# Optimization experiments

Hardware: AMD Instinct MI355X
Metric: run time of the kernel (lower is better)

Reference implementation:

```python
import jax, jax.numpy as jnp
import numpy as np
import math

HEAD_DIM = 64
EMBED_DIM = 512
B, T = 16, 2048

def setup_inputs() -> dict:
    key = jax.random.key(0)
    k1, k2, k3 = jax.random.split(key, 3)
    x = jax.random.normal(k1, (B, T, EMBED_DIM), dtype=jnp.float32)
    # nn.Linear-style init scale
    s = 1.0 / math.sqrt(EMBED_DIM)
    Wq = jax.random.uniform(k2, (EMBED_DIM, HEAD_DIM), dtype=jnp.float32, minval=-s, maxval=s)
    bq = jax.random.uniform(k3, (HEAD_DIM,), dtype=jnp.float32, minval=-s, maxval=s)
    return {"x": x, "Wq": Wq, "bq": bq}

def reference(x, Wq, bq):
    # Faithful to source: q, k, v all come from the SAME query projection.
    q = jnp.einsum('bte,ed->btd', x, Wq) + bq  # [B,T,D]
    d_k = q.shape[-1]
    # weights[b, i, j] = q_i . q_j / sqrt(d_k)
    weights = jnp.einsum('bid,bjd->bij', q, q) / jnp.sqrt(jnp.float32(d_k))
    # NOTE: source applies softmax over dim=1 (query/row axis), not dim=-1.
    weights = jax.nn.softmax(weights, axis=1)
    attention = jnp.einsum('bij,bjd->bid', weights, q)  # v == q in source
    return attention
```

## Files before the change

kernel.cpp:

```cpp
#include <hip/hip_runtime.h>
#include <hip/hip_bf16.h>

#define BN 16
#define TN 2048
#define DN 64
#define EN 512
#define PAD 68

using f32x4  = __attribute__((ext_vector_type(4))) float;
using bf16x8 = __attribute__((ext_vector_type(8))) short;
using bf16x4 = __attribute__((ext_vector_type(4))) short;

static __device__ __forceinline__ short f2bf(float f) {
    __hip_bfloat16 h = __float2bfloat16(f);
    return __builtin_bit_cast(short, h);
}
static __device__ __forceinline__ float bf2f(short s) {
    return __bfloat162float(__builtin_bit_cast(__hip_bfloat16, s));
}

__global__ __launch_bounds__(256) void wprep_kernel(
    const float* __restrict__ Wq, short* __restrict__ WTh,
    short* __restrict__ WTl)
{
    __shared__ float wlds[64][65];
    const int tid = threadIdx.x;
    const int k0 = blockIdx.x * 64;
    #pragma unroll
    for (int it = 0; it < 16; ++it) {
        int idx = it * 256 + tid;
        int k = idx >> 6, n = idx & 63;
        wlds[k][n] = Wq[(size_t)(k0 + k) * 64 + n];
    }
    __syncthreads();
    #pragma unroll
    for (int it = 0; it < 16; ++it) {
        int idx = it * 256 + tid;
        int n = idx >> 6, k = idx & 63;
        float v = wlds[k][n];
        short h = f2bf(v);
        short l = f2bf(v - bf2f(h));
        WTh[(size_t)n * EN + k0 + k] = h;
        WTl[(size_t)n * EN + k0 + k] = l;
    }
}

__global__ __launch_bounds__(256, 2) void qproj_kernel(
    const float* __restrict__ x, const short* __restrict__ WTh,
    const short* __restrict__ WTl, const float* __restrict__ bq,
    short* __restrict__ Qb, short* __restrict__ QTb)
{
    __shared__ short xh[64 * 40];
    __shared__ short wth[64 * 40];
    __shared__ short wtl[64 * 40];
    __shared__ short tl[64][68];

    const int tid = threadIdx.x;
    const int lane = tid & 63;
    const int wv = tid >> 6;
    const int c = lane & 15;
    const int g = lane >> 4;
    const int rowbase = blockIdx.x * 64;
    const int b = rowbase >> 11;
    const int tbase = rowbase & (TN - 1);

    const int sr = tid >> 3;
    const int sc4 = tid & 7;

    float4 xa = *reinterpret_cast<const float4*>(&x[(size_t)(rowbase + sr) * EN + sc4 * 4]);
    float4 xb = *reinterpret_cast<const float4*>(&x[(size_t)(rowbase + 32 + sr) * EN + sc4 * 4]);
    bf16x4 wa = *reinterpret_cast<const bf16x4*>(&WTh[(size_t)sr * EN + sc4 * 4]);
    bf16x4 wb = *reinterpret_cast<const bf16x4*>(&WTh[(size_t)(32 + sr) * EN + sc4 * 4]);
    bf16x4 la = *reinterpret_cast<const bf16x4*>(&WTl[(size_t)sr * EN + sc4 * 4]);
    bf16x4 lb = *reinterpret_cast<const bf16x4*>(&WTl[(size_t)(32 + sr) * EN + sc4 * 4]);

    f32x4 acc[4];
    #pragma unroll
    for (int nt = 0; nt < 4; ++nt) acc[nt] = (f32x4){0.f, 0.f, 0.f, 0.f};

    for (int ks = 0; ks < EN; ks += 32) {
        __syncthreads();
        bf16x4 h0, h1;
        #pragma unroll
        for (int j = 0; j < 4; ++j) { h0[j] = f2bf(xa[j]); h1[j] = f2bf(xb[j]); }
        *reinterpret_cast<bf16x4*>(&xh[sr * 40 + sc4 * 4]) = h0;
        *reinterpret_cast<bf16x4*>(&xh[(32 + sr) * 40 + sc4 * 4]) = h1;
        *reinterpret_cast<bf16x4*>(&wth[sr * 40 + sc4 * 4]) = wa;
        *reinterpret_cast<bf16x4*>(&wth[(32 + sr) * 40 + sc4 * 4]) = wb;
        *reinterpret_cast<bf16x4*>(&wtl[sr * 40 + sc4 * 4]) = la;
        *reinterpret_cast<bf16x4*>(&wtl[(32 + sr) * 40 + sc4 * 4]) = lb;

        const int kn = (ks + 32 < EN) ? ks + 32 : ks;
        xa = *reinterpret_cast<const float4*>(&x[(size_t)(rowbase + sr) * EN + kn + sc4 * 4]);
        xb = *reinterpret_cast<const float4*>(&x[(size_t)(rowbase + 32 + sr) * EN + kn + sc4 * 4]);
        wa = *reinterpret_cast<const bf16x4*>(&WTh[(size_t)sr * EN + kn + sc4 * 4]);
        wb = *reinterpret_cast<const bf16x4*>(&WTh[(size_t)(32 + sr) * EN + kn + sc4 * 4]);
        la = *reinterpret_cast<const bf16x4*>(&WTl[(size_t)sr * EN + kn + sc4 * 4]);
        lb = *reinterpret_cast<const bf16x4*>(&WTl[(size_t)(32 + sr) * EN + kn + sc4 * 4]);
        __syncthreads();

        bf16x8 av = *reinterpret_cast<const bf16x8*>(&xh[(wv * 16 + c) * 40 + g * 8]);
        #pragma unroll
        for (int nt = 0; nt < 4; ++nt) {
            bf16x8 bh = *reinterpret_cast<const bf16x8*>(&wth[(nt * 16 + c) * 40 + g * 8]);
            bf16x8 bl = *reinterpret_cast<const bf16x8*>(&wtl[(nt * 16 + c) * 40 + g * 8]);
            acc[nt] = __builtin_amdgcn_mfma_f32_16x16x32_bf16(av, bh, acc[nt], 0, 0, 0);
            acc[nt] = __builtin_amdgcn_mfma_f32_16x16x32_bf16(av, bl, acc[nt], 0, 0, 0);
        }
    }

    __syncthreads();
    #pragma unroll
    for (int nt = 0; nt < 4; ++nt) {
        const float bias = bq[nt * 16 + c];
        #pragma unroll
        for (int r = 0; r < 4; ++r) {
            const int row = wv * 16 + g * 4 + r;
            short qb = f2bf(acc[nt][r] + bias);
            Qb[(size_t)(rowbase + row) * DN + nt * 16 + c] = qb;
            tl[nt * 16 + c][row] = qb;
        }
    }
    __syncthreads();
    #pragma unroll
    for (int it = 0; it < 4; ++it) {
        int idx = it * 256 + tid;
        int d = idx >> 4;
        int j4 = (idx & 15) * 4;
        *reinterpret_cast<short4*>(&QTb[((size_t)(b * 64 + d)) * TN + tbase + j4]) =
            *reinterpret_cast<const short4*>(&tl[d][j4]);
    }
}

__global__ __launch_bounds__(256, 4) void stats_kernel(
    const short* __restrict__ Qb, float* __restrict__ l_part)
{
    __shared__ short Qt[64 * PAD];
    const int tid = threadIdx.x;
    const int lane = tid & 63;
    const int wv = tid >> 6;
    const int c = lane & 15;
    const int g = lane >> 4;
    const int b = blockIdx.y;
    const int z = blockIdx.z;
    const int jbase = blockIdx.x * 64 + wv * 16;
    const short* Qbb = Qb + (size_t)b * TN * DN;

    bf16x8 a0 = *reinterpret_cast<const bf16x8*>(Qbb + (size_t)(jbase + c) * DN + g * 8);
    bf16x8 a1 = *reinterpret_cast<const bf16x8*>(Qbb + (size_t)(jbase + c) * DN + g * 8 + 32);

    const int srow = tid >> 2;
    const int schk = tid & 3;
    const int ilo = z * (TN / 2);

    bf16x8 v0 = *reinterpret_cast<const bf16x8*>(Qbb + (size_t)(ilo + srow) * DN + schk * 16);
    bf16x8 v1 = *reinterpret_cast<const bf16x8*>(Qbb + (size_t)(ilo + srow) * DN + schk * 16 + 8);

    float l[4] = {0.f, 0.f, 0.f, 0.f};
    for (int ii = 0; ii < TN / 2; ii += 64) {
        __syncthreads();
        *reinterpret_cast<bf16x8*>(&Qt[srow * PAD + schk * 16]) = v0;
        *reinterpret_cast<bf16x8*>(&Qt[srow * PAD + schk * 16 + 8]) = v1;
        const int in_ = ilo + ((ii + 64 < TN / 2) ? ii + 64 : ii);
        v0 = *reinterpret_cast<const bf16x8*>(Qbb + (size_t)(in_ + srow) * DN + schk * 16);
        v1 = *reinterpret_cast<const bf16x8*>(Qbb + (size_t)(in_ + srow) * DN + schk * 16 + 8);
        __syncthreads();

        #pragma unroll
        for (int it = 0; it < 4; ++it) {
            bf16x8 b0 = *reinterpret_cast<const bf16x8*>(&Qt[(it * 16 + c) * PAD + g * 8]);
            bf16x8 b1 = *reinterpret_cast<const bf16x8*>(&Qt[(it * 16 + c) * PAD + g * 8 + 32]);
            f32x4 acc = {0.f, 0.f, 0.f, 0.f};
            acc = __builtin_amdgcn_mfma_f32_16x16x32_bf16(a0, b0, acc, 0, 0, 0);
            acc = __builtin_amdgcn_mfma_f32_16x16x32_bf16(a1, b1, acc, 0, 0, 0);
            #pragma unroll
            for (int r = 0; r < 4; ++r)
                l[r] += __expf(acc[r] * 0.125f);
        }
    }
    #pragma unroll
    for (int r = 0; r < 4; ++r) {
        float v = l[r];
        v += __shfl_xor(v, 1);
        v += __shfl_xor(v, 2);
        v += __shfl_xor(v, 4);
        v += __shfl_xor(v, 8);
        l[r] = v;
    }
    if (c == 0) {
        #pragma unroll
        for (int r = 0; r < 4; ++r)
            l_part[((size_t)z * BN + b) * TN + jbase + g * 4 + r] = l[r];
    }
}

__global__ __launch_bounds__(256) void fuse_kernel(
    const short* __restrict__ QTb, const float* __restrict__ l_part,
    short* __restrict__ RT)
{
    const int idx = blockIdx.x * 256 + threadIdx.x;
    const int c8 = idx & 255;
    const int bd = idx >> 8;
    const int b = bd >> 6;
    const int j0 = c8 * 8;

    bf16x8 q = *reinterpret_cast<const bf16x8*>(&QTb[(size_t)bd * TN + j0]);
    const float* lp0 = l_part + (size_t)b * TN + j0;
    const float* lp1 = l_part + (size_t)(BN + b) * TN + j0;
    bf16x8 r;
    #pragma unroll
    for (int t = 0; t < 8; ++t)
        r[t] = f2bf(bf2f(q[t]) / (lp0[t] + lp1[t]));
    *reinterpret_cast<bf16x8*>(&RT[(size_t)bd * TN + j0]) = r;
}

__global__ __launch_bounds__(256, 4) void pv_kernel(
    const short* __restrict__ Qb, const short* __restrict__ RT,
    float* __restrict__ out0, float* __restrict__ out1)
{
    __shared__ short Qt[64 * PAD];
    __shared__ short RTt[64 * PAD];
    __shared__ short Pt[4][16 * PAD];

    const int tid = threadIdx.x;
    const int lane = tid & 63;
    const int wv = tid >> 6;
    const int c = lane & 15;
    const int g = lane >> 4;
    const int b = blockIdx.y;
    const int z = blockIdx.z;
    const int ibase = blockIdx.x * 64 + wv * 16;
    const short* Qbb = Qb + (size_t)b * TN * DN;
    const short* RTb = RT + (size_t)b * DN * TN;

    bf16x8 bi0 = *reinterpret_cast<const bf16x8*>(Qbb + (size_t)(ibase + c) * DN + g * 8);
    bf16x8 bi1 = *reinterpret_cast<const bf16x8*>(Qbb + (size_t)(ibase + c) * DN + g * 8 + 32);

    f32x4 o[4];
    #pragma unroll
    for (int dt = 0; dt < 4; ++dt) o[dt] = (f32x4){0.f, 0.f, 0.f, 0.f};

    const int srow = tid >> 2;
    const int schk = tid & 3;
    const int jlo = z * (TN / 2);

    bf16x8 vq0 = *reinterpret_cast<const bf16x8*>(Qbb + (size_t)(jlo + srow) * DN + schk * 16);
    bf16x8 vq1 = *reinterpret_cast<const bf16x8*>(Qbb + (size_t)(jlo + srow) * DN + schk * 16 + 8);
    bf16x8 vt0 = *reinterpret_cast<const bf16x8*>(RTb + (size_t)srow * TN + jlo + schk * 16);
    bf16x8 vt1 = *reinterpret_cast<const bf16x8*>(RTb + (size_t)srow * TN + jlo + schk * 16 + 8);

    for (int jj = 0; jj < TN / 2; jj += 64) {
        __syncthreads();
        *reinterpret_cast<bf16x8*>(&Qt[srow * PAD + schk * 16]) = vq0;
        *reinterpret_cast<bf16x8*>(&Qt[srow * PAD + schk * 16 + 8]) = vq1;
        *reinterpret_cast<bf16x8*>(&RTt[srow * PAD + schk * 16]) = vt0;
        *reinterpret_cast<bf16x8*>(&RTt[srow * PAD + schk * 16 + 8]) = vt1;

        const int jn = jlo + ((jj + 64 < TN / 2) ? jj + 64 : jj);
        vq0 = *reinterpret_cast<const bf16x8*>(Qbb + (size_t)(jn + srow) * DN + schk * 16);
        vq1 = *reinterpret_cast<const bf16x8*>(Qbb + (size_t)(jn + srow) * DN + schk * 16 + 8);
        vt0 = *reinterpret_cast<const bf16x8*>(RTb + (size_t)srow * TN + jn + schk * 16);
        vt1 = *reinterpret_cast<const bf16x8*>(RTb + (size_t)srow * TN + jn + schk * 16 + 8);
        __syncthreads();

        bf16x8 aq[4][2];
        #pragma unroll
        for (int dt = 0; dt < 4; ++dt) {
            aq[dt][0] = *reinterpret_cast<const bf16x8*>(&RTt[(dt * 16 + c) * PAD + g * 8]);
            aq[dt][1] = *reinterpret_cast<const bf16x8*>(&RTt[(dt * 16 + c) * PAD + 32 + g * 8]);
        }

        #pragma unroll
        for (int jt = 0; jt < 4; ++jt) {
            bf16x8 a0 = *reinterpret_cast<const bf16x8*>(&Qt[(jt * 16 + c) * PAD + g * 8]);
            bf16x8 a1 = *reinterpret_cast<const bf16x8*>(&Qt[(jt * 16 + c) * PAD + g * 8 + 32]);
            f32x4 accs = {0.f, 0.f, 0.f, 0.f};
            accs = __builtin_amdgcn_mfma_f32_16x16x32_bf16(a0, bi0, accs, 0, 0, 0);
            accs = __builtin_amdgcn_mfma_f32_16x16x32_bf16(a1, bi1, accs, 0, 0, 0);
            bf16x4 pw;
            #pragma unroll
            for (int r = 0; r < 4; ++r)
                pw[r] = f2bf(__expf(accs[r] * 0.125f));
            *reinterpret_cast<bf16x4*>(&Pt[wv][c * PAD + jt * 16 + g * 4]) = pw;
        }
        asm volatile("s_waitcnt lgkmcnt(0)" ::: "memory");
        __builtin_amdgcn_sched_barrier(0);

        bf16x8 p0 = *reinterpret_cast<const bf16x8*>(&Pt[wv][c * PAD + g * 8]);
        bf16x8 p1 = *reinterpret_cast<const bf16x8*>(&Pt[wv][c * PAD + 32 + g * 8]);
        #pragma unroll
        for (int dt = 0; dt < 4; ++dt) {
            o[dt] = __builtin_amdgcn_mfma_f32_16x16x32_bf16(aq[dt][0], p0, o[dt], 0, 0, 0);
            o[dt] = __builtin_amdgcn_mfma_f32_16x16x32_bf16(aq[dt][1], p1, o[dt], 0, 0, 0);
        }
    }

    float* outb = (z ? out1 : out0) + (size_t)b * TN * DN;
    #pragma unroll
    for (int dt = 0; dt < 4; ++dt) {
        float4 v4;
        v4.x = o[dt][0]; v4.y = o[dt][1]; v4.z = o[dt][2]; v4.w = o[dt][3];
        *reinterpret_cast<float4*>(&outb[(size_t)(ibase + c) * DN + dt * 16 + g * 4]) = v4;
    }
}

__global__ __launch_bounds__(256) void reduce_kernel(
    float* __restrict__ out, const float* __restrict__ part1)
{
    const size_t i = (size_t)blockIdx.x * 256 + threadIdx.x;
    float4 a = reinterpret_cast<float4*>(out)[i];
    float4 b = reinterpret_cast<const float4*>(part1)[i];
    a.x += b.x; a.y += b.y; a.z += b.z; a.w += b.w;
    reinterpret_cast<float4*>(out)[i] = a;
}

extern "C" void kernel_launch(void* const* d_in, const int* in_sizes, int n_in,
                              void* d_out, int out_size, void* d_ws, size_t ws_size,
                              hipStream_t stream) {
    const float* x  = (const float*)d_in[0];
    const float* Wq = (const float*)d_in[1];
    const float* bq = (const float*)d_in[2];
    float* out = (float*)d_out;

    short* Qb   = (short*)d_ws;
    short* QTb  = Qb + (size_t)BN * TN * DN;
    short* RT   = QTb + (size_t)BN * TN * DN;
    float* lpar = (float*)(RT + (size_t)BN * TN * DN);
    short* WTh  = (short*)(lpar + (size_t)2 * BN * TN);
    short* WTl  = WTh + (size_t)DN * EN;
    float* part1 = (float*)(WTl + (size_t)DN * EN);

    wprep_kernel<<<dim3(EN / 64), dim3(256), 0, stream>>>(Wq, WTh, WTl);
    qproj_kernel<<<dim3(BN * TN / 64), dim3(256), 0, stream>>>(x, WTh, WTl, bq, Qb, QTb);
    stats_kernel<<<dim3(TN / 64, BN, 2), dim3(256), 0, stream>>>(Qb, lpar);
    fuse_kernel<<<dim3(BN * DN * TN / 8 / 256), dim3(256), 0, stream>>>(QTb, lpar, RT);
    pv_kernel<<<dim3(TN / 64, BN, 2), dim3(256), 0, stream>>>(Qb, RT, out, part1);
    reduce_kernel<<<dim3(BN * TN * DN / 4 / 256), dim3(256), 0, stream>>>(out, part1);
}
```

Measured before the change: 82.49 us.

## Double-buffer qproj LDS, fold exp scale into Q, split stats four ways

The Q projection kernel now double-buffers its LDS tiles, so each k-step needs one barrier instead of two, and global loads are issued two steps ahead. The 1/sqrt(d)*log2(e) factor is folded into the stored Qb so the exponentials become plain exp2 with no multiply. The stats kernel is split four ways along the sum axis to give more blocks, and the fuse kernel now sums four partial denominators. __syncthreads is replaced by a lighter lgkmcnt wait plus s_barrier. This adds LDS use and partial-sum traffic, and rounding Q after scaling changes numerics slightly.

```diff
diff --git a/kernel.cpp b/kernel.cpp
--- a/kernel.cpp
+++ b/kernel.cpp
@@ -6,6 +6,7 @@
 #define DN 64
 #define EN 512
 #define PAD 68
+#define SQK 0.42466084f
 
 using f32x4  = __attribute__((ext_vector_type(4))) float;
 using bf16x8 = __attribute__((ext_vector_type(8))) short;
@@ -17,6 +18,10 @@
 }
 static __device__ __forceinline__ float bf2f(short s) {
     return __bfloat162float(__builtin_bit_cast(__hip_bfloat16, s));
+}
+static __device__ __forceinline__ void bar_lds() {
+    asm volatile("s_waitcnt lgkmcnt(0)" ::: "memory");
+    __builtin_amdgcn_s_barrier();
 }
 
 __global__ __launch_bounds__(256) void wprep_kernel(
@@ -50,9 +55,9 @@
     const short* __restrict__ WTl, const float* __restrict__ bq,
     short* __restrict__ Qb, short* __restrict__ QTb)
 {
-    __shared__ short xh[64 * 40];
-    __shared__ short wth[64 * 40];
-    __shared__ short wtl[64 * 40];
+    __shared__ short xh[2 * 64 * 40];
+    __shared__ short wth[2 * 64 * 40];
+    __shared__ short wtl[2 * 64 * 40];
     __shared__ short tl[64][68];
 
     const int tid = threadIdx.x;
@@ -66,20 +71,21 @@
 
     const int sr = tid >> 3;
     const int sc4 = tid & 7;
-
-    float4 xa = *reinterpret_cast<const float4*>(&x[(size_t)(rowbase + sr) * EN + sc4 * 4]);
-    float4 xb = *reinterpret_cast<const float4*>(&x[(size_t)(rowbase + 32 + sr) * EN + sc4 * 4]);
-    bf16x4 wa = *reinterpret_cast<const bf16x4*>(&WTh[(size_t)sr * EN + sc4 * 4]);
-    bf16x4 wb = *reinterpret_cast<const bf16x4*>(&WTh[(size_t)(32 + sr) * EN + sc4 * 4]);
-    bf16x4 la = *reinterpret_cast<const bf16x4*>(&WTl[(size_t)sr * EN + sc4 * 4]);
-    bf16x4 lb = *reinterpret_cast<const bf16x4*>(&WTl[(size_t)(32 + sr) * EN + sc4 * 4]);
-
-    f32x4 acc[4];
-    #pragma unroll
-    for (int nt = 0; nt < 4; ++nt) acc[nt] = (f32x4){0.f, 0.f, 0.f, 0.f};
-
-    for (int ks = 0; ks < EN; ks += 32) {
-        __syncthreads();
+    const size_t xr0 = (size_t)(rowbase + sr) * EN + sc4 * 4;
+    const size_t xr1 = (size_t)(rowbase + 32 + sr) * EN + sc4 * 4;
+    const size_t wr0 = (size_t)sr * EN + sc4 * 4;
+    const size_t wr1 = (size_t)(32 + sr) * EN + sc4 * 4;
+
+    float4 xa, xb;
+    bf16x4 wa, wb, la, lb;
+
+    xa = *reinterpret_cast<const float4*>(&x[xr0]);
+    xb = *reinterpret_cast<const float4*>(&x[xr1]);
+    wa = *reinterpret_cast<const bf16x4*>(&WTh[wr0]);
+    wb = *reinterpret_cast<const bf16x4*>(&WTh[wr1]);
+    la = *reinterpret_cast<const bf16x4*>(&WTl[wr0]);
+    lb = *reinterpret_cast<const bf16x4*>(&WTl[wr1]);
+    {
         bf16x4 h0, h1;
         #pragma unroll
         for (int j = 0; j < 4; ++j) { h0[j] = f2bf(xa[j]); h1[j] = f2bf(xb[j]); }
@@ -89,24 +95,53 @@
         *reinterpret_cast<bf16x4*>(&wth[(32 + sr) * 40 + sc4 * 4]) = wb;
         *reinterpret_cast<bf16x4*>(&wtl[sr * 40 + sc4 * 4]) = la;
         *reinterpret_cast<bf16x4*>(&wtl[(32 + sr) * 40 + sc4 * 4]) = lb;
-
-        const int kn = (ks + 32 < EN) ? ks + 32 : ks;
-        xa = *reinterpret_cast<const float4*>(&x[(size_t)(rowbase + sr) * EN + kn + sc4 * 4]);
-        xb = *reinterpret_cast<const float4*>(&x[(size_t)(rowbase + 32 + sr) * EN + kn + sc4 * 4]);
-        wa = *reinterpret_cast<const bf16x4*>(&WTh[(size_t)sr * EN + kn + sc4 * 4]);
-        wb = *reinterpret_cast<const bf16x4*>(&WTh[(size_t)(32 + sr) * EN + kn + sc4 * 4]);
-        la = *reinterpret_cast<const bf16x4*>(&WTl[(size_t)sr * EN + kn + sc4 * 4]);
-        lb = *reinterpret_cast<const bf16x4*>(&WTl[(size_t)(32 + sr) * EN + kn + sc4 * 4]);
-        __syncthreads();
-
-        bf16x8 av = *reinterpret_cast<const bf16x8*>(&xh[(wv * 16 + c) * 40 + g * 8]);
+    }
+    xa = *reinterpret_cast<const float4*>(&x[xr0 + 32]);
+    xb = *reinterpret_cast<const float4*>(&x[xr1 + 32]);
+    wa = *reinterpret_cast<const bf16x4*>(&WTh[wr0 + 32]);
+    wb = *reinterpret_cast<const bf16x4*>(&WTh[wr1 + 32]);
+    la = *reinterpret_cast<const bf16x4*>(&WTl[wr0 + 32]);
+    lb = *reinterpret_cast<const bf16x4*>(&WTl[wr1 + 32]);
+    bar_lds();
+
+    f32x4 acc[4];
+    #pragma unroll
+    for (int nt = 0; nt < 4; ++nt) acc[nt] = (f32x4){0.f, 0.f, 0.f, 0.f};
+
+    for (int t = 0; t < 16; ++t) {
+        const int cur = t & 1;
+        const int co = cur * 2560;
+        if (t + 1 < 16) {
+            const int wo = (cur ^ 1) * 2560;
+            bf16x4 h0, h1;
+            #pragma unroll
+            for (int j = 0; j < 4; ++j) { h0[j] = f2bf(xa[j]); h1[j] = f2bf(xb[j]); }
+            *reinterpret_cast<bf16x4*>(&xh[wo + sr * 40 + sc4 * 4]) = h0;
+            *reinterpret_cast<bf16x4*>(&xh[wo + (32 + sr) * 40 + sc4 * 4]) = h1;
+            *reinterpret_cast<bf16x4*>(&wth[wo + sr * 40 + sc4 * 4]) = wa;
+            *reinterpret_cast<bf16x4*>(&wth[wo + (32 + sr) * 40 + sc4 * 4]) = wb;
+            *reinterpret_cast<bf16x4*>(&wtl[wo + sr * 40 + sc4 * 4]) = la;
+            *reinterpret_cast<bf16x4*>(&wtl[wo + (32 + sr) * 40 + sc4 * 4]) = lb;
+        }
+        if (t + 2 < 16) {
+            const int kn = (t + 2) * 32;
+            xa = *reinterpret_cast<const float4*>(&x[xr0 + kn]);
+            xb = *reinterpret_cast<const float4*>(&x[xr1 + kn]);
+            wa = *reinterpret_cast<const bf16x4*>(&WTh[wr0 + kn]);
+            wb = *reinterpret_cast<const bf16x4*>(&WTh[wr1 + kn]);
+            la = *reinterpret_cast<const bf16x4*>(&WTl[wr0 + kn]);
+            lb = *reinterpret_cast<const bf16x4*>(&WTl[wr1 + kn]);
+        }
+
+        bf16x8 av = *reinterpret_cast<const bf16x8*>(&xh[co + (wv * 16 + c) * 40 + g * 8]);
         #pragma unroll
         for (int nt = 0; nt < 4; ++nt) {
-            bf16x8 bh = *reinterpret_cast<const bf16x8*>(&wth[(nt * 16 + c) * 40 + g * 8]);
-            bf16x8 bl = *reinterpret_cast<const bf16x8*>(&wtl[(nt * 16 + c) * 40 + g * 8]);
+            bf16x8 bh = *reinterpret_cast<const bf16x8*>(&wth[co + (nt * 16 + c) * 40 + g * 8]);
+            bf16x8 bl = *reinterpret_cast<const bf16x8*>(&wtl[co + (nt * 16 + c) * 40 + g * 8]);
             acc[nt] = __builtin_amdgcn_mfma_f32_16x16x32_bf16(av, bh, acc[nt], 0, 0, 0);
             acc[nt] = __builtin_amdgcn_mfma_f32_16x16x32_bf16(av, bl, acc[nt], 0, 0, 0);
         }
+        bar_lds();
     }
 
     __syncthreads();
@@ -116,9 +151,9 @@
         #pragma unroll
         for (int r = 0; r < 4; ++r) {
             const int row = wv * 16 + g * 4 + r;
-            short qb = f2bf(acc[nt][r] + bias);
-            Qb[(size_t)(rowbase + row) * DN + nt * 16 + c] = qb;
-            tl[nt * 16 + c][row] = qb;
+            const float q = acc[nt][r] + bias;
+            Qb[(size_t)(rowbase + row) * DN + nt * 16 + c] = f2bf(q * SQK);
+            tl[nt * 16 + c][row] = f2bf(q);
         }
     }
     __syncthreads();
@@ -151,20 +186,20 @@
 
     const int srow = tid >> 2;
     const int schk = tid & 3;
-    const int ilo = z * (TN / 2);
+    const int ilo = z * (TN / 4);
 
     bf16x8 v0 = *reinterpret_cast<const bf16x8*>(Qbb + (size_t)(ilo + srow) * DN + schk * 16);
     bf16x8 v1 = *reinterpret_cast<const bf16x8*>(Qbb + (size_t)(ilo + srow) * DN + schk * 16 + 8);
 
     float l[4] = {0.f, 0.f, 0.f, 0.f};
-    for (int ii = 0; ii < TN / 2; ii += 64) {
-        __syncthreads();
+    for (int ii = 0; ii < TN / 4; ii += 64) {
+        bar_lds();
         *reinterpret_cast<bf16x8*>(&Qt[srow * PAD + schk * 16]) = v0;
         *reinterpret_cast<bf16x8*>(&Qt[srow * PAD + schk * 16 + 8]) = v1;
-        const int in_ = ilo + ((ii + 64 < TN / 2) ? ii + 64 : ii);
+        const int in_ = ilo + ((ii + 64 < TN / 4) ? ii + 64 : ii);
         v0 = *reinterpret_cast<const bf16x8*>(Qbb + (size_t)(in_ + srow) * DN + schk * 16);
         v1 = *reinterpret_cast<const bf16x8*>(Qbb + (size_t)(in_ + srow) * DN + schk * 16 + 8);
-        __syncthreads();
+        bar_lds();
 
         #pragma unroll
         for (int it = 0; it < 4; ++it) {
@@ -175,7 +210,7 @@
             acc = __builtin_amdgcn_mfma_f32_16x16x32_bf16(a1, b1, acc, 0, 0, 0);
             #pragma unroll
             for (int r = 0; r < 4; ++r)
-                l[r] += __expf(acc[r] * 0.125f);
+                l[r] += __builtin_exp2f(acc[r]);
         }
     }
     #pragma unroll
@@ -207,10 +242,12 @@
     bf16x8 q = *reinterpret_cast<const bf16x8*>(&QTb[(size_t)bd * TN + j0]);
     const float* lp0 = l_part + (size_t)b * TN + j0;
     const float* lp1 = l_part + (size_t)(BN + b) * TN + j0;
+    const float* lp2 = l_part + (size_t)(2 * BN + b) * TN + j0;
+    const float* lp3 = l_part + (size_t)(3 * BN + b) * TN + j0;
     bf16x8 r;
     #pragma unroll
     for (int t = 0; t < 8; ++t)
-        r[t] = f2bf(bf2f(q[t]) / (lp0[t] + lp1[t]));
+        r[t] = f2bf(bf2f(q[t]) / (lp0[t] + lp1[t] + lp2[t] + lp3[t]));
     *reinterpret_cast<bf16x8*>(&RT[(size_t)bd * TN + j0]) = r;
 }
 
@@ -250,7 +287,7 @@
     bf16x8 vt1 = *reinterpret_cast<const bf16x8*>(RTb + (size_t)srow * TN + jlo + schk * 16 + 8);
 
     for (int jj = 0; jj < TN / 2; jj += 64) {
-        __syncthreads();
+        bar_lds();
         *reinterpret_cast<bf16x8*>(&Qt[srow * PAD + schk * 16]) = vq0;
         *reinterpret_cast<bf16x8*>(&Qt[srow * PAD + schk * 16 + 8]) = vq1;
         *reinterpret_cast<bf16x8*>(&RTt[srow * PAD + schk * 16]) = vt0;
@@ -261,7 +298,7 @@
         vq1 = *reinterpret_cast<const bf16x8*>(Qbb + (size_t)(jn + srow) * DN + schk * 16 + 8);
         vt0 = *reinterpret_cast<const bf16x8*>(RTb + (size_t)srow * TN + jn + schk * 16);
         vt1 = *reinterpret_cast<const bf16x8*>(RTb + (size_t)srow * TN + jn + schk * 16 + 8);
-        __syncthreads();
+        bar_lds();
 
         bf16x8 aq[4][2];
         #pragma unroll
@@ -280,7 +317,7 @@
             bf16x4 pw;
             #pragma unroll
             for (int r = 0; r < 4; ++r)
-                pw[r] = f2bf(__expf(accs[r] * 0.125f));
+                pw[r] = f2bf(__builtin_exp2f(accs[r]));
             *reinterpret_cast<bf16x4*>(&Pt[wv][c * PAD + jt * 16 + g * 4]) = pw;
         }
         asm volatile("s_waitcnt lgkmcnt(0)" ::: "memory");
@@ -326,13 +363,13 @@
     short* QTb  = Qb + (size_t)BN * TN * DN;
     short* RT   = QTb + (size_t)BN * TN * DN;
     float* lpar = (float*)(RT + (size_t)BN * TN * DN);
-    short* WTh  = (short*)(lpar + (size_t)2 * BN * TN);
+    short* WTh  = (short*)(lpar + (size_t)4 * BN * TN);
     short* WTl  = WTh + (size_t)DN * EN;
     float* part1 = (float*)(WTl + (size_t)DN * EN);
 
     wprep_kernel<<<dim3(EN / 64), dim3(256), 0, stream>>>(Wq, WTh, WTl);
     qproj_kernel<<<dim3(BN * TN / 64), dim3(256), 0, stream>>>(x, WTh, WTl, bq, Qb, QTb);
-    stats_kernel<<<dim3(TN / 64, BN, 2), dim3(256), 0, stream>>>(Qb, lpar);
+    stats_kernel<<<dim3(TN / 64, BN, 4), dim3(256), 0, stream>>>(Qb, lpar);
     fuse_kernel<<<dim3(BN * DN * TN / 8 / 256), dim3(256), 0, stream>>>(QTb, lpar, RT);
     pv_kernel<<<dim3(TN / 64, BN, 2), dim3(256), 0, stream>>>(Qb, RT, out, part1);
     reduce_kernel<<<dim3(BN * TN * DN / 4 / 256), dim3(256), 0, stream>>>(out, part1);
```

Measured after the change: 89.27 us. +8.2%, slower.
